# Kernel optimization log

Measured on AMD Instinct MI355X. Metric: run time of the kernel, lower is better.

## Reference

```python
import jax, jax.numpy as jnp
import numpy as np

D_MODEL = 2048
NUM_HEADS = 16
D_K = D_MODEL // NUM_HEADS  # 128
BATCH, SEQ = 2, 2048


def setup_inputs() -> dict:
    key = jax.random.key(0)
    ks = jax.random.split(key, 9)
    s = 0.02
    return {
        "x": jax.random.normal(ks[0], (BATCH, SEQ, D_MODEL), dtype=jnp.float32),
        "W_q": jax.random.normal(ks[1], (D_MODEL, D_MODEL), dtype=jnp.float32) * s,
        "b_q": jax.random.normal(ks[2], (D_MODEL,), dtype=jnp.float32) * s,
        "W_k": jax.random.normal(ks[3], (D_MODEL, D_K), dtype=jnp.float32) * s,
        "b_k": jax.random.normal(ks[4], (D_K,), dtype=jnp.float32) * s,
        "W_v": jax.random.normal(ks[5], (D_MODEL, D_K), dtype=jnp.float32) * s,
        "b_v": jax.random.normal(ks[6], (D_K,), dtype=jnp.float32) * s,
        "W_o": jax.random.normal(ks[7], (D_MODEL, D_MODEL), dtype=jnp.float32) * s,
        "b_o": jax.random.normal(ks[8], (D_MODEL,), dtype=jnp.float32) * s,
    }


def reference(x, W_q, b_q, W_k, b_k, W_v, b_v, W_o, b_o):
    B, S, _ = x.shape
    # Q: per-head projections -> (B, H, S, d_k)
    Q = (x @ W_q + b_q).reshape(B, S, NUM_HEADS, D_K).transpose(0, 2, 1, 3)
    # K, V: single shared head -> (B, S, d_k)
    K = x @ W_k + b_k
    V = x @ W_v + b_v
    scale = 1.0 / np.sqrt(D_K)
    # scores: (B, H, S_q, S_k); K broadcast across heads (no expand materialized)
    scores = jnp.einsum("bhqd,bkd->bhqk", Q, K) * scale
    attn = jax.nn.softmax(scores, axis=-1)
    out = jnp.einsum("bhqk,bkd->bhqd", attn, V)  # (B, H, S, d_k)
    out = out.transpose(0, 2, 1, 3).reshape(B, S, D_MODEL)
    out = out @ W_o + b_o
    K_cache = K[:, None, :, :]  # (B, 1, S, d_k)
    V_cache = V[:, None, :, :]
    return (out, K_cache, V_cache)
```

## Files before the change

### kernel.cpp

```cpp
#include <hip/hip_runtime.h>
#include <cstdint>

typedef __bf16 bf16x8 __attribute__((ext_vector_type(8)));
typedef float f32x4 __attribute__((ext_vector_type(4)));
typedef unsigned short ushort_t;

constexpr int kS  = 2048;
constexpr int kDM = 2048;
constexpr int kDK = 128;
constexpr int kNH = 16;
constexpr int kB  = 2;
constexpr int kNQKV = kDM + 2 * kDK;

__device__ __forceinline__ unsigned short f2bf(float f) {
  union { float f; unsigned u; } v; v.f = f;
  unsigned u = v.u;
  u += 0x7fffu + ((u >> 16) & 1u);
  return (unsigned short)(u >> 16);
}

__device__ __forceinline__ void gload16(const void* g, void* l) {
  __builtin_amdgcn_global_load_lds(
      (const __attribute__((address_space(1))) void*)g,
      (__attribute__((address_space(3))) void*)l, 16, 0, 0);
}

__device__ __forceinline__ void xcd_swizzle(int& bx, int& by) {
  int gx = gridDim.x;
  int nwg = gx * gridDim.y;
  int id = by * gx + bx;
  int cpx = nwg >> 3;
  int sw = (id & 7) * cpx + (id >> 3);
  bx = sw % gx;
  by = sw / gx;
}

__global__ __launch_bounds__(256) void cast_f32_bf16(const float* __restrict__ in,
                                                     ushort_t* __restrict__ out, long n) {
  long i = ((long)blockIdx.x * 256 + threadIdx.x) * 4;
  if (i >= n) return;
  float4 f = *reinterpret_cast<const float4*>(in + i);
  ushort4 o;
  o.x = f2bf(f.x); o.y = f2bf(f.y); o.z = f2bf(f.z); o.w = f2bf(f.w);
  *reinterpret_cast<ushort4*>(out + i) = o;
}

__global__ __launch_bounds__(256) void transpose_cast(const float* __restrict__ in,
                                                      ushort_t* __restrict__ out,
                                                      int R, int C) {
  __shared__ float tile[32][33];
  int c = blockIdx.x * 32 + threadIdx.x;
  int r0 = blockIdx.y * 32;
  #pragma unroll
  for (int i = threadIdx.y; i < 32; i += 8)
    tile[i][threadIdx.x] = in[(long)(r0 + i) * C + c];
  __syncthreads();
  int oc  = r0 + threadIdx.x;
  int or0 = blockIdx.x * 32;
  #pragma unroll
  for (int i = threadIdx.y; i < 32; i += 8)
    out[(long)(or0 + i) * R + oc] = f2bf(tile[threadIdx.x][i]);
}

__device__ __forceinline__ void gemm128(const ushort_t* __restrict__ A, int lda,
                                        const ushort_t* __restrict__ Bt, int ldb,
                                        int K, int row0, int col0,
                                        f32x4 (&acc)[4][4]) {
  __shared__ __align__(16) ushort_t sA[2][128 * 32];
  __shared__ __align__(16) ushort_t sB[2][128 * 32];
  int t = threadIdx.x;
  int r = t >> 2, c4 = t & 3;
  const ushort_t* gA0 = A  + (long)(row0 + r)      * lda + c4 * 8;
  const ushort_t* gA1 = A  + (long)(row0 + r + 64) * lda + c4 * 8;
  const ushort_t* gB0 = Bt + (long)(col0 + r)      * ldb + c4 * 8;
  const ushort_t* gB1 = Bt + (long)(col0 + r + 64) * ldb + c4 * 8;
  int lane = t & 63, wave = t >> 6;
  int wr = wave >> 1, wc = wave & 1;
  int lr = lane & 15, lg = lane >> 4;
  int aoff = (wr * 64 + lr) * 32 + lg * 8;
  int boff = (wc * 64 + lr) * 32 + lg * 8;

  auto stage = [&](int kk, int bb) {
    gload16(gA0 + kk, (void*)(sA[bb] + t * 8));
    gload16(gA1 + kk, (void*)(sA[bb] + 2048 + t * 8));
    gload16(gB0 + kk, (void*)(sB[bb] + t * 8));
    gload16(gB1 + kk, (void*)(sB[bb] + 2048 + t * 8));
  };
  auto comp = [&](int bb) {
    bf16x8 af[4], bg[4];
    #pragma unroll
    for (int i = 0; i < 4; i++) af[i] = *(const bf16x8*)(sA[bb] + aoff + i * 16 * 32);
    #pragma unroll
    for (int j = 0; j < 4; j++) bg[j] = *(const bf16x8*)(sB[bb] + boff + j * 16 * 32);
    #pragma unroll
    for (int i = 0; i < 4; i++)
      #pragma unroll
      for (int j = 0; j < 4; j++)
        acc[i][j] = __builtin_amdgcn_mfma_f32_16x16x32_bf16(af[i], bg[j], acc[i][j], 0, 0, 0);
  };

  stage(0, 0);
  __syncthreads();
  for (int kk = 0; kk < K; kk += 64) {
    stage(kk + 32, 1);
    comp(0);
    __syncthreads();
    if (kk + 64 < K) stage(kk + 64, 0);
    comp(1);
    __syncthreads();
  }
}

__global__ __launch_bounds__(256) void gemm_qkv(const ushort_t* __restrict__ x,
    const ushort_t* __restrict__ Wt, const float* __restrict__ bq,
    const float* __restrict__ bk, const float* __restrict__ bv,
    ushort_t* __restrict__ Qb, float* __restrict__ Kc,
    ushort_t* __restrict__ Kb, float* __restrict__ Vc, ushort_t* __restrict__ Vtb) {
  f32x4 acc[4][4] = {};
  int bx = blockIdx.x, by = blockIdx.y;
  xcd_swizzle(bx, by);
  int row0 = by * 128, col0 = bx * 128;
  gemm128(x, kDM, Wt, kDM, kDM, row0, col0, acc);
  int lane = threadIdx.x & 63, wave = threadIdx.x >> 6;
  int wr = wave >> 1, wc = wave & 1, lr = lane & 15, lg = lane >> 4;
  #pragma unroll
  for (int i = 0; i < 4; i++) {
    #pragma unroll
    for (int j = 0; j < 4; j++) {
      int col = col0 + wc * 64 + j * 16 + lr;
      float bias = (col < kDM) ? bq[col]
                 : (col < kDM + kDK) ? bk[col - kDM] : bv[col - kDM - kDK];
      #pragma unroll
      for (int rr = 0; rr < 4; rr++) {
        int row = row0 + wr * 64 + i * 16 + lg * 4 + rr;
        float v = acc[i][j][rr] + bias;
        if (col < kDM) {
          Qb[(long)row * kDM + col] = f2bf(v);
        } else if (col < kDM + kDK) {
          int c = col - kDM;
          Kc[(long)row * kDK + c] = v;
          Kb[(long)row * kDK + c] = f2bf(v);
        } else {
          int c = col - kDM - kDK;
          Vc[(long)row * kDK + c] = v;
          Vtb[((long)(row >> 11) * kDK + c) * kS + (row & 2047)] = f2bf(v);
        }
      }
    }
  }
}

__global__ __launch_bounds__(256) void gemm_out(const ushort_t* __restrict__ A,
    const ushort_t* __restrict__ Wt, const float* __restrict__ bias,
    float* __restrict__ C) {
  f32x4 acc[4][4] = {};
  int bx = blockIdx.x, by = blockIdx.y;
  xcd_swizzle(bx, by);
  int row0 = by * 128, col0 = bx * 128;
  gemm128(A, kDM, Wt, kDM, kDM, row0, col0, acc);
  int lane = threadIdx.x & 63, wave = threadIdx.x >> 6;
  int wr = wave >> 1, wc = wave & 1, lr = lane & 15, lg = lane >> 4;
  #pragma unroll
  for (int i = 0; i < 4; i++) {
    #pragma unroll
    for (int j = 0; j < 4; j++) {
      int col = col0 + wc * 64 + j * 16 + lr;
      float bv = bias[col];
      #pragma unroll
      for (int rr = 0; rr < 4; rr++) {
        int row = row0 + wr * 64 + i * 16 + lg * 4 + rr;
        C[(long)row * kDM + col] = acc[i][j][rr] + bv;
      }
    }
  }
}

__global__ __launch_bounds__(512, 2) void flash_attn(
    const ushort_t* __restrict__ Qb, const ushort_t* __restrict__ Kb,
    const ushort_t* __restrict__ Vt, ushort_t* __restrict__ Ob) {
  __shared__ __align__(16) ushort_t sK[2][64 * 128];
  __shared__ __align__(16) ushort_t sV[2][64 * 128];

  const int tid = threadIdx.x;
  const int L = tid & 63, wave = tid >> 6;
  const int lr = L & 15, lg = L >> 4;
  const int b = blockIdx.y >> 1, hg = blockIdx.y & 1;
  const int h = hg * 8 + wave;
  const int q0 = blockIdx.x * 32;

  const ushort_t* Kg = Kb + (long)b * kS * kDK;
  const ushort_t* Vg = Vt + (long)b * kDK * kS;
  const ushort_t* Qg = Qb + ((long)b * kS + q0) * kDM + h * kDK;

  bf16x8 qf[2][4];
  #pragma unroll
  for (int i = 0; i < 2; i++)
    #pragma unroll
    for (int kk = 0; kk < 4; kk++)
      qf[i][kk] = *(const bf16x8*)(Qg + (long)(i * 16 + lr) * kDM + kk * 32 + lg * 8);

  int koff[2], voff[2];
  #pragma unroll
  for (int s = 0; s < 2; s++) {
    int c = tid + s * 512;
    int f = c >> 6, cl = c & 63;
    int st = f >> 2, kk = f & 3, n = cl & 15;
    int key = (st >> 1) * 32 + (n >> 2) * 8 + (st & 1) * 4 + (n & 3);
    koff[s] = key * kDK + kk * 32 + (cl >> 4) * 8;
    int d = c >> 3, kb = (c & 7) ^ (d & 7);
    voff[s] = d * kS + kb * 8;
  }

  f32x4 accO[8][2] = {};
  float lsum[2] = {};

  constexpr float kScaleLog2e = 0.12751743f;

  auto stage = [&](int jt, int bb) {
    const ushort_t* Kt = Kg + (long)jt * 64 * kDK;
    const ushort_t* Vtg = Vg + jt * 64;
    #pragma unroll
    for (int s = 0; s < 2; s++) {
      int c8 = (tid + s * 512) * 8;
      gload16(Kt + koff[s], (void*)(sK[bb] + c8));
      gload16(Vtg + voff[s], (void*)(sV[bb] + c8));
    }
  };

  auto compute = [&](int bb) {
    #pragma unroll
    for (int u = 0; u < 2; u++) {
      f32x4 sacc[2][2] = {};
      __builtin_amdgcn_s_setprio(1);
      #pragma unroll
      for (int kk = 0; kk < 4; kk++)
        #pragma unroll
        for (int jj = 0; jj < 2; jj++) {
          bf16x8 kf = *(const bf16x8*)(sK[bb] + ((u * 2 + jj) * 4 + kk) * 512 + L * 8);
          #pragma unroll
          for (int i = 0; i < 2; i++)
            sacc[jj][i] = __builtin_amdgcn_mfma_f32_16x16x32_bf16(kf, qf[i][kk], sacc[jj][i], 0, 0, 0);
        }
      __builtin_amdgcn_s_setprio(0);

      bf16x8 pf[2];
      #pragma unroll
      for (int i = 0; i < 2; i++) {
        union { bf16x8 v; unsigned w[4]; } P;
        #pragma unroll
        for (int jj = 0; jj < 2; jj++) {
          float p0 = __builtin_amdgcn_exp2f(sacc[jj][i][0] * kScaleLog2e);
          float p1 = __builtin_amdgcn_exp2f(sacc[jj][i][1] * kScaleLog2e);
          float p2 = __builtin_amdgcn_exp2f(sacc[jj][i][2] * kScaleLog2e);
          float p3 = __builtin_amdgcn_exp2f(sacc[jj][i][3] * kScaleLog2e);
          lsum[i] += (p0 + p1) + (p2 + p3);
          asm("v_cvt_pk_bf16_f32 %0, %1, %2" : "=v"(P.w[jj * 2 + 0]) : "v"(p0), "v"(p1));
          asm("v_cvt_pk_bf16_f32 %0, %1, %2" : "=v"(P.w[jj * 2 + 1]) : "v"(p2), "v"(p3));
        }
        pf[i] = P.v;
      }

      __builtin_amdgcn_s_setprio(1);
      #pragma unroll
      for (int t = 0; t < 8; t++) {
        int kbL = (u * 4 + lg) ^ (lr & 7);
        bf16x8 vf = *(const bf16x8*)(sV[bb] + t * 1024 + lr * 64 + kbL * 8);
        #pragma unroll
        for (int i = 0; i < 2; i++)
          accO[t][i] = __builtin_amdgcn_mfma_f32_16x16x32_bf16(vf, pf[i], accO[t][i], 0, 0, 0);
      }
      __builtin_amdgcn_s_setprio(0);
    }
  };

  stage(0, 0);
  __syncthreads();
  for (int jt = 0; jt < 32; jt += 2) {
    stage(jt + 1, 1);
    compute(0);
    __syncthreads();
    if (jt + 2 < 32) stage(jt + 2, 0);
    compute(1);
    __syncthreads();
  }

  float inv[2];
  #pragma unroll
  for (int i = 0; i < 2; i++) {
    float v = lsum[i];
    v += __shfl_xor(v, 16);
    v += __shfl_xor(v, 32);
    inv[i] = 1.0f / v;
  }

  ushort_t* Og = Ob + ((long)b * kS + q0) * kDM + h * kDK;
  #pragma unroll
  for (int t = 0; t < 8; t++)
    #pragma unroll
    for (int i = 0; i < 2; i++) {
      union { ushort4 o; unsigned w[2]; } O;
      float f0 = accO[t][i][0] * inv[i];
      float f1 = accO[t][i][1] * inv[i];
      float f2 = accO[t][i][2] * inv[i];
      float f3 = accO[t][i][3] * inv[i];
      asm("v_cvt_pk_bf16_f32 %0, %1, %2" : "=v"(O.w[0]) : "v"(f0), "v"(f1));
      asm("v_cvt_pk_bf16_f32 %0, %1, %2" : "=v"(O.w[1]) : "v"(f2), "v"(f3));
      *(ushort4*)(Og + (long)(i * 16 + lr) * kDM + t * 16 + lg * 4) = O.o;
    }
}

extern "C" void kernel_launch(void* const* d_in, const int* in_sizes, int n_in,
                              void* d_out, int out_size, void* d_ws, size_t ws_size,
                              hipStream_t stream) {
  (void)in_sizes; (void)n_in; (void)out_size; (void)ws_size;
  const float* x   = (const float*)d_in[0];
  const float* W_q = (const float*)d_in[1];
  const float* b_q = (const float*)d_in[2];
  const float* W_k = (const float*)d_in[3];
  const float* b_k = (const float*)d_in[4];
  const float* W_v = (const float*)d_in[5];
  const float* b_v = (const float*)d_in[6];
  const float* W_o = (const float*)d_in[7];
  const float* b_o = (const float*)d_in[8];

  float* out = (float*)d_out;
  float* Kc  = out + (long)kB * kS * kDM;
  float* Vc  = Kc  + (long)kB * kS * kDK;

  char* w = (char*)d_ws;
  ushort_t* x_bf   = (ushort_t*)w;  w += 16777216;
  ushort_t* Wall_t = (ushort_t*)w;  w += (size_t)kNQKV*kDM*2;
  ushort_t* Wo_t   = (ushort_t*)w;  w += 8388608;
  ushort_t* Q_bf   = (ushort_t*)w;  w += 16777216;
  ushort_t* K_bf   = (ushort_t*)w;  w += 1048576;
  ushort_t* Vt_bf  = (ushort_t*)w;  w += 1048576;
  ushort_t* O_bf   = (ushort_t*)w;  w += 16777216;

  dim3 blk(256);
  dim3 tblk(32, 8);

  cast_f32_bf16<<<dim3(8192), blk, 0, stream>>>(x, x_bf, (long)kB * kS * kDM);
  transpose_cast<<<dim3(64, 64), tblk, 0, stream>>>(W_q, Wall_t, kDM, kDM);
  transpose_cast<<<dim3(4, 64),  tblk, 0, stream>>>(W_k, Wall_t + (long)kDM * kDM, kDM, kDK);
  transpose_cast<<<dim3(4, 64),  tblk, 0, stream>>>(W_v, Wall_t + (long)(kDM + kDK) * kDM, kDM, kDK);
  transpose_cast<<<dim3(64, 64), tblk, 0, stream>>>(W_o, Wo_t, kDM, kDM);

  gemm_qkv<<<dim3(kNQKV / 128, kB * kS / 128), blk, 0, stream>>>(
      x_bf, Wall_t, b_q, b_k, b_v, Q_bf, Kc, K_bf, Vc, Vt_bf);

  flash_attn<<<dim3(kS / 32, kB * 2), dim3(512), 0, stream>>>(Q_bf, K_bf, Vt_bf, O_bf);

  gemm_out<<<dim3(kDM / 128, kB * kS / 128), blk, 0, stream>>>(O_bf, Wo_t, b_o, out);
}
```

Baseline: 311.5 us.

## Fuse weight-prep kernels into one launch and shrink GEMM tiles to 128x64

Merges the x cast and the four weight transpose-casts into a single `prep` kernel that dispatches on block index, replacing five launches with one. Both projection GEMMs switch from 128x128 to 128x64 output tiles, which doubles the block count. The goal is better CU occupancy and less tail imbalance on the many-CU device, at the cost of lower operand reuse per block and more redundant A-tile loads.

```diff
diff --git a/kernel.cpp b/kernel.cpp
--- a/kernel.cpp
+++ b/kernel.cpp
@@ -35,67 +35,74 @@
   by = sw / gx;
 }
 
-__global__ __launch_bounds__(256) void cast_f32_bf16(const float* __restrict__ in,
-                                                     ushort_t* __restrict__ out, long n) {
-  long i = ((long)blockIdx.x * 256 + threadIdx.x) * 4;
-  if (i >= n) return;
-  float4 f = *reinterpret_cast<const float4*>(in + i);
-  ushort4 o;
-  o.x = f2bf(f.x); o.y = f2bf(f.y); o.z = f2bf(f.z); o.w = f2bf(f.w);
-  *reinterpret_cast<ushort4*>(out + i) = o;
-}
-
-__global__ __launch_bounds__(256) void transpose_cast(const float* __restrict__ in,
-                                                      ushort_t* __restrict__ out,
-                                                      int R, int C) {
+__global__ __launch_bounds__(256) void prep(
+    const float* __restrict__ x, ushort_t* __restrict__ x_bf,
+    const float* __restrict__ Wq, const float* __restrict__ Wk,
+    const float* __restrict__ Wv, const float* __restrict__ Wo,
+    ushort_t* __restrict__ Wall_t, ushort_t* __restrict__ Wo_t) {
   __shared__ float tile[32][33];
-  int c = blockIdx.x * 32 + threadIdx.x;
-  int r0 = blockIdx.y * 32;
-  #pragma unroll
-  for (int i = threadIdx.y; i < 32; i += 8)
-    tile[i][threadIdx.x] = in[(long)(r0 + i) * C + c];
+  int bid = blockIdx.x, tid = threadIdx.x;
+  if (bid < 8192) {
+    long i = ((long)bid * 256 + tid) * 4;
+    float4 f = *reinterpret_cast<const float4*>(x + i);
+    ushort4 o;
+    o.x = f2bf(f.x); o.y = f2bf(f.y); o.z = f2bf(f.z); o.w = f2bf(f.w);
+    *reinterpret_cast<ushort4*>(x_bf + i) = o;
+    return;
+  }
+  int id = bid - 8192;
+  const float* in; ushort_t* out; int C, bx, by;
+  const int R = 2048;
+  if (id < 4096)      { in = Wq; out = Wall_t;                      C = 2048; bx = id & 63; by = id >> 6; }
+  else if (id < 4352) { id -= 4096; in = Wk; out = Wall_t + (long)kDM * kDM;            C = 128; bx = id & 3; by = id >> 2; }
+  else if (id < 4608) { id -= 4352; in = Wv; out = Wall_t + (long)(kDM + kDK) * kDM;    C = 128; bx = id & 3; by = id >> 2; }
+  else                { id -= 4608; in = Wo; out = Wo_t;            C = 2048; bx = id & 63; by = id >> 6; }
+  int tx = tid & 31, ty = tid >> 5;
+  int c = bx * 32 + tx;
+  int r0 = by * 32;
+  #pragma unroll
+  for (int i = ty; i < 32; i += 8)
+    tile[i][tx] = in[(long)(r0 + i) * C + c];
   __syncthreads();
-  int oc  = r0 + threadIdx.x;
-  int or0 = blockIdx.x * 32;
-  #pragma unroll
-  for (int i = threadIdx.y; i < 32; i += 8)
-    out[(long)(or0 + i) * R + oc] = f2bf(tile[threadIdx.x][i]);
-}
-
-__device__ __forceinline__ void gemm128(const ushort_t* __restrict__ A, int lda,
-                                        const ushort_t* __restrict__ Bt, int ldb,
-                                        int K, int row0, int col0,
-                                        f32x4 (&acc)[4][4]) {
+  int oc  = r0 + tx;
+  int or0 = bx * 32;
+  #pragma unroll
+  for (int i = ty; i < 32; i += 8)
+    out[(long)(or0 + i) * R + oc] = f2bf(tile[tx][i]);
+}
+
+__device__ __forceinline__ void gemm128x64(const ushort_t* __restrict__ A, int lda,
+                                           const ushort_t* __restrict__ Bt, int ldb,
+                                           int K, int row0, int col0,
+                                           f32x4 (&acc)[4][2]) {
   __shared__ __align__(16) ushort_t sA[2][128 * 32];
-  __shared__ __align__(16) ushort_t sB[2][128 * 32];
+  __shared__ __align__(16) ushort_t sB[2][64 * 32];
   int t = threadIdx.x;
   int r = t >> 2, c4 = t & 3;
   const ushort_t* gA0 = A  + (long)(row0 + r)      * lda + c4 * 8;
   const ushort_t* gA1 = A  + (long)(row0 + r + 64) * lda + c4 * 8;
   const ushort_t* gB0 = Bt + (long)(col0 + r)      * ldb + c4 * 8;
-  const ushort_t* gB1 = Bt + (long)(col0 + r + 64) * ldb + c4 * 8;
   int lane = t & 63, wave = t >> 6;
   int wr = wave >> 1, wc = wave & 1;
   int lr = lane & 15, lg = lane >> 4;
   int aoff = (wr * 64 + lr) * 32 + lg * 8;
-  int boff = (wc * 64 + lr) * 32 + lg * 8;
+  int boff = (wc * 32 + lr) * 32 + lg * 8;
 
   auto stage = [&](int kk, int bb) {
     gload16(gA0 + kk, (void*)(sA[bb] + t * 8));
     gload16(gA1 + kk, (void*)(sA[bb] + 2048 + t * 8));
     gload16(gB0 + kk, (void*)(sB[bb] + t * 8));
-    gload16(gB1 + kk, (void*)(sB[bb] + 2048 + t * 8));
   };
   auto comp = [&](int bb) {
-    bf16x8 af[4], bg[4];
+    bf16x8 af[4], bg[2];
     #pragma unroll
     for (int i = 0; i < 4; i++) af[i] = *(const bf16x8*)(sA[bb] + aoff + i * 16 * 32);
     #pragma unroll
-    for (int j = 0; j < 4; j++) bg[j] = *(const bf16x8*)(sB[bb] + boff + j * 16 * 32);
+    for (int j = 0; j < 2; j++) bg[j] = *(const bf16x8*)(sB[bb] + boff + j * 16 * 32);
     #pragma unroll
     for (int i = 0; i < 4; i++)
       #pragma unroll
-      for (int j = 0; j < 4; j++)
+      for (int j = 0; j < 2; j++)
         acc[i][j] = __builtin_amdgcn_mfma_f32_16x16x32_bf16(af[i], bg[j], acc[i][j], 0, 0, 0);
   };
 
@@ -116,18 +123,18 @@
     const float* __restrict__ bk, const float* __restrict__ bv,
     ushort_t* __restrict__ Qb, float* __restrict__ Kc,
     ushort_t* __restrict__ Kb, float* __restrict__ Vc, ushort_t* __restrict__ Vtb) {
-  f32x4 acc[4][4] = {};
+  f32x4 acc[4][2] = {};
   int bx = blockIdx.x, by = blockIdx.y;
   xcd_swizzle(bx, by);
-  int row0 = by * 128, col0 = bx * 128;
-  gemm128(x, kDM, Wt, kDM, kDM, row0, col0, acc);
+  int row0 = by * 128, col0 = bx * 64;
+  gemm128x64(x, kDM, Wt, kDM, kDM, row0, col0, acc);
   int lane = threadIdx.x & 63, wave = threadIdx.x >> 6;
   int wr = wave >> 1, wc = wave & 1, lr = lane & 15, lg = lane >> 4;
   #pragma unroll
   for (int i = 0; i < 4; i++) {
     #pragma unroll
-    for (int j = 0; j < 4; j++) {
-      int col = col0 + wc * 64 + j * 16 + lr;
+    for (int j = 0; j < 2; j++) {
+      int col = col0 + wc * 32 + j * 16 + lr;
       float bias = (col < kDM) ? bq[col]
                  : (col < kDM + kDK) ? bk[col - kDM] : bv[col - kDM - kDK];
       #pragma unroll
@@ -153,18 +160,18 @@
 __global__ __launch_bounds__(256) void gemm_out(const ushort_t* __restrict__ A,
     const ushort_t* __restrict__ Wt, const float* __restrict__ bias,
     float* __restrict__ C) {
-  f32x4 acc[4][4] = {};
+  f32x4 acc[4][2] = {};
   int bx = blockIdx.x, by = blockIdx.y;
   xcd_swizzle(bx, by);
-  int row0 = by * 128, col0 = bx * 128;
-  gemm128(A, kDM, Wt, kDM, kDM, row0, col0, acc);
+  int row0 = by * 128, col0 = bx * 64;
+  gemm128x64(A, kDM, Wt, kDM, kDM, row0, col0, acc);
   int lane = threadIdx.x & 63, wave = threadIdx.x >> 6;
   int wr = wave >> 1, wc = wave & 1, lr = lane & 15, lg = lane >> 4;
   #pragma unroll
   for (int i = 0; i < 4; i++) {
     #pragma unroll
-    for (int j = 0; j < 4; j++) {
-      int col = col0 + wc * 64 + j * 16 + lr;
+    for (int j = 0; j < 2; j++) {
+      int col = col0 + wc * 32 + j * 16 + lr;
       float bv = bias[col];
       #pragma unroll
       for (int rr = 0; rr < 4; rr++) {
@@ -337,18 +344,13 @@
   ushort_t* O_bf   = (ushort_t*)w;  w += 16777216;
 
   dim3 blk(256);
-  dim3 tblk(32, 8);
-
-  cast_f32_bf16<<<dim3(8192), blk, 0, stream>>>(x, x_bf, (long)kB * kS * kDM);
-  transpose_cast<<<dim3(64, 64), tblk, 0, stream>>>(W_q, Wall_t, kDM, kDM);
-  transpose_cast<<<dim3(4, 64),  tblk, 0, stream>>>(W_k, Wall_t + (long)kDM * kDM, kDM, kDK);
-  transpose_cast<<<dim3(4, 64),  tblk, 0, stream>>>(W_v, Wall_t + (long)(kDM + kDK) * kDM, kDM, kDK);
-  transpose_cast<<<dim3(64, 64), tblk, 0, stream>>>(W_o, Wo_t, kDM, kDM);
-
-  gemm_qkv<<<dim3(kNQKV / 128, kB * kS / 128), blk, 0, stream>>>(
+
+  prep<<<dim3(16896), blk, 0, stream>>>(x, x_bf, W_q, W_k, W_v, W_o, Wall_t, Wo_t);
+
+  gemm_qkv<<<dim3(kNQKV / 64, kB * kS / 128), blk, 0, stream>>>(
       x_bf, Wall_t, b_q, b_k, b_v, Q_bf, Kc, K_bf, Vc, Vt_bf);
 
   flash_attn<<<dim3(kS / 32, kB * 2), dim3(512), 0, stream>>>(Q_bf, K_bf, Vt_bf, O_bf);
 
-  gemm_out<<<dim3(kDM / 128, kB * kS / 128), blk, 0, stream>>>(O_bf, Wo_t, b_o, out);
-}
+  gemm_out<<<dim3(kDM / 64, kB * kS / 128), blk, 0, stream>>>(O_bf, Wo_t, b_o, out);
+}
```

Result: slower. 336.2 us (+7.9%).
